# Performance work log

Measured on AMD Instinct MI355X. Metric: run time of the kernel, lower is better.

The kernel has to match this reference:

```python
import jax, jax.numpy as jnp
import numpy as np


def _conv(x, w):
    # 3x3 conv, stride 1, pad 1, NCHW / OIHW
    return jax.lax.conv_general_dilated(
        x, w, window_strides=(1, 1), padding=[(1, 1), (1, 1)],
        dimension_numbers=("NCHW", "OIHW", "NCHW"))


def _up2(x):
    return jnp.repeat(jnp.repeat(x, 2, axis=2), 2, axis=3)


def setup_inputs() -> dict:
    key = jax.random.key(0)
    ks = jax.random.split(key, 16)
    B, S = 8, 256
    d = {
        "x": jax.random.normal(ks[0], (B, 256, 64, 64), jnp.float32),
        "enc1": jax.random.normal(ks[1], (B, 64, 256, 256), jnp.float32),
        "enc2": jax.random.normal(ks[2], (B, 128, 128, 128), jnp.float32),
        "enc3": jax.random.normal(ks[3], (B, 256, 64, 64), jnp.float32),
        "style": jax.random.normal(ks[4], (B, S), jnp.float32),
        # modconv1: 512 -> 128 (bias unused in original F.conv2d call)
        "w1": jax.random.normal(ks[5], (128, 512, 3, 3), jnp.float32) * 0.02,
        "fc_w1": jax.random.normal(ks[6], (128, S), jnp.float32) * 0.05,
        "fc_b1": jax.random.normal(ks[7], (128,), jnp.float32) * 0.05,
        # modconv2: 256 -> 64
        "w2": jax.random.normal(ks[8], (64, 256, 3, 3), jnp.float32) * 0.02,
        "fc_w2": jax.random.normal(ks[9], (64, S), jnp.float32) * 0.05,
        "fc_b2": jax.random.normal(ks[10], (64,), jnp.float32) * 0.05,
        # final_conv: 128 -> 64 -> 3, with biases
        "fw1": jax.random.normal(ks[11], (64, 128, 3, 3), jnp.float32) * 0.02,
        "fb1": jax.random.normal(ks[12], (64,), jnp.float32) * 0.02,
        "fw2": jax.random.normal(ks[13], (3, 64, 3, 3), jnp.float32) * 0.02,
        "fb2": jax.random.normal(ks[14], (3,), jnp.float32) * 0.02,
    }
    return d


def _modconv(x, style, w, fc_w, fc_b):
    # style modulation scales each OUTPUT channel of the conv weight:
    # conv(x, w * s[o]) == s[o] * conv(x, w)  (linearity), so fuse into a
    # single batched conv followed by a per-channel scale.
    s = style @ fc_w.T + fc_b          # [B, out_ch]
    return _conv(x, w) * s[:, :, None, None]


def reference(x, enc1, enc2, enc3, style,
              w1, fc_w1, fc_b1, w2, fc_w2, fc_b2,
              fw1, fb1, fw2, fb2):
    h = jnp.concatenate([x, enc3], axis=1)            # [B,512,64,64]
    h = _up2(h)                                       # [B,512,128,128]
    h = jax.nn.relu(_modconv(h, style, w1, fc_w1, fc_b1))  # [B,128,128,128]
    h = jnp.concatenate([h, enc2], axis=1)            # [B,256,128,128]
    h = _up2(h)                                       # [B,256,256,256]
    h = jax.nn.relu(_modconv(h, style, w2, fc_w2, fc_b2))  # [B,64,256,256]
    h = jnp.concatenate([h, enc1], axis=1)            # [B,128,256,256]
    h = jax.nn.relu(_conv(h, fw1) + fb1[None, :, None, None])
    h = _conv(h, fw2) + fb2[None, :, None, None]      # [B,3,256,256]
    return h
```

## Files before the change

kernel.cpp:

```cpp
#include <hip/hip_runtime.h>
#include <hip/hip_bf16.h>
#include <cstdint>
#include <cstddef>

typedef short short8 __attribute__((ext_vector_type(8)));
typedef unsigned short ushort8 __attribute__((ext_vector_type(8)));
typedef float f32x4 __attribute__((ext_vector_type(4)));

#define DI __device__ __forceinline__

DI float bf2f(__hip_bfloat16 h) { return __bfloat162float(h); }
DI unsigned short f2bf(float f) {
    __hip_bfloat16 h = __float2bfloat16(f);
    return *(unsigned short*)&h;
}

constexpr int cilog2(int v) { int r = 0; while (v > 1) { v >>= 1; ++r; } return r; }

__global__ void detect_dtype(const unsigned short* __restrict__ raw,
                             int* __restrict__ flag) {
    __shared__ int cnt;
    if (threadIdx.x == 0) cnt = 0;
    __syncthreads();
    int local = 0;
    for (int i = threadIdx.x; i < 1024; i += 256) {
        unsigned short u = raw[2 * i];
        int e = (u >> 7) & 0xFF;
        if (e >= 110 && e <= 132) local++;
    }
    atomicAdd(&cnt, local);
    __syncthreads();
    if (threadIdx.x == 0) *flag = (cnt < 512) ? 1 : 0;
}

__global__ void cvt_pad_f32(const void* __restrict__ in, float* __restrict__ out,
                            int n, int npad, const int* __restrict__ flag) {
    int i = blockIdx.x * blockDim.x + threadIdx.x;
    if (i >= npad) return;
    float v = 0.f;
    if (i < n) v = (*flag) ? ((const float*)in)[i] : bf2f(((const __hip_bfloat16*)in)[i]);
    out[i] = v;
}

__global__ void style_mod(const void* __restrict__ style, const void* __restrict__ fcw,
                          const void* __restrict__ fcb, float* __restrict__ out,
                          int B, int O, int S, const int* __restrict__ flag) {
    int i = blockIdx.x * blockDim.x + threadIdx.x;
    if (i >= B * O) return;
    int b = i / O, o = i - b * O;
    float acc = 0.f;
    if (*flag) {
        const float* sp = (const float*)style + (size_t)b * S;
        const float* wp = (const float*)fcw + (size_t)o * S;
        for (int k = 0; k < S; ++k) acc = fmaf(sp[k], wp[k], acc);
        acc += ((const float*)fcb)[o];
    } else {
        const __hip_bfloat16* sp = (const __hip_bfloat16*)style + (size_t)b * S;
        const __hip_bfloat16* wp = (const __hip_bfloat16*)fcw + (size_t)o * S;
        for (int k = 0; k < S; ++k) acc = fmaf(bf2f(sp[k]), bf2f(wp[k]), acc);
        acc += bf2f(((const __hip_bfloat16*)fcb)[o]);
    }
    out[i] = acc;
}

__global__ __launch_bounds__(256)
void nchw_to_nhwc(const void* __restrict__ in, unsigned short* __restrict__ out,
                  int C, int HW, int CT, int coff, const int* __restrict__ flag) {
    __shared__ float t[32][65];
    const int f32 = flag[0];
    const int pbase = blockIdx.x * 64;
    const int cbase = blockIdx.y * 32;
    const int b = blockIdx.z;
    const size_t ibase = ((size_t)b * C + cbase) * HW + pbase;
#pragma unroll
    for (int i = 0; i < 8; ++i) {
        int e = threadIdx.x + i * 256;
        int c = e >> 6, p = e & 63;
        size_t idx = ibase + (size_t)c * HW + p;
        float v = f32 ? ((const float*)in)[idx] : bf2f(((const __hip_bfloat16*)in)[idx]);
        t[c][p] = v;
    }
    __syncthreads();
#pragma unroll
    for (int i = 0; i < 8; ++i) {
        int e = threadIdx.x + i * 256;
        int p = e >> 5, c = e & 31;
        out[((size_t)b * HW + pbase + p) * CT + coff + cbase + c] = f2bf(t[c][p]);
    }
}

__global__ __launch_bounds__(256)
void pack_w(const void* __restrict__ w, unsigned short* __restrict__ pkw,
            int Creal, int CIN, int NC, int KC, const int* __restrict__ flag) {
    int gid = blockIdx.x * 256 + threadIdx.x;
    int total = 9 * KC * NC * 64;
    if (gid >= total) return;
    const int f32 = flag[0];
    int lane = gid & 63; int q = gid >> 6;
    int nc = q % NC; q /= NC; int tap = q % 9; int kc = q / 9;
    int lm = lane & 15, lk = lane >> 4;
    int n = nc * 16 + lm;
    int kh = tap / 3, kw = tap - kh * 3;
    ushort8 v;
#pragma unroll
    for (int j = 0; j < 8; ++j) {
        int k = kc * 32 + lk * 8 + j;
        float f = 0.f;
        if (n < Creal) {
            size_t si = (((size_t)n * CIN + k) * 3 + kh) * 3 + kw;
            f = f32 ? ((const float*)w)[si] : bf2f(((const __hip_bfloat16*)w)[si]);
        }
        v[j] = f2bf(f);
    }
    *(ushort8*)(pkw + (size_t)gid * 8) = v;
}

template<int CT, int H, int W, bool UP, int NT, int NCT, int EPI, int CTO>
__global__ __launch_bounds__(256, 3)
void conv_tile(const unsigned short* __restrict__ in,
               const unsigned short* __restrict__ pkw,
               const float* __restrict__ sb,
               unsigned short* __restrict__ outp) {
    constexpr int KC = CT / 32;
    constexpr int SH = UP ? H / 2 : H;
    constexpr int SW = UP ? W / 2 : W;
    constexpr int NROW = UP ? 6 : 10;
    constexpr int NCOL = UP ? 18 : 34;
    constexpr int NPIX = NROW * NCOL;
    constexpr int NUNIT = 4 * NPIX;
    constexpr int TILES_X = W / 32;
    constexpr int DCOL = UP ? 8 : 16;

    __shared__ __align__(16) unsigned short inA[NUNIT * 8];
    __shared__ __align__(16) unsigned short wbuf[9 * NT * 512];

    const int tid = threadIdx.x;
    const int wave = tid >> 6, lane = tid & 63;
    const int lm = lane & 15, lk = lane >> 4;
    const int x0 = (blockIdx.x % TILES_X) * 32;
    const int y0 = (blockIdx.x / TILES_X) * 8;
    const int nco0 = blockIdx.y * NT;
    const int b = blockIdx.z;

    const int sy0 = UP ? ((y0 - 1) >> 1) : (y0 - 1);
    const int sx0 = UP ? ((x0 - 1) >> 1) : (x0 - 1);

    const unsigned short* gin = in + (size_t)b * SH * SW * CT;

    f32x4 acc[4][NT];
#pragma unroll
    for (int t = 0; t < 4; ++t)
#pragma unroll
        for (int u = 0; u < NT; ++u)
            acc[t][u] = f32x4{0.f, 0.f, 0.f, 0.f};

    for (int kc = 0; kc < KC; ++kc) {
        __syncthreads();
        for (int u0 = tid; u0 < NUNIT; u0 += 256) {
            int pix = u0 >> 2, j = u0 & 3;
            int sr = pix / NCOL, sc = pix - sr * NCOL;
            int gy = sy0 + sr, gx = sx0 + sc;
            uint4 v = uint4{0u, 0u, 0u, 0u};
            if (gy >= 0 && gy < SH && gx >= 0 && gx < SW)
                v = *(const uint4*)((const char*)gin +
                      ((size_t)(gy * SW + gx) * CT + kc * 32) * 2 + j * 16);
            *(uint4*)((char*)inA + (((j * NROW + sr) * NCOL + sc) << 4)) = v;
        }
        {
            const char* wsrc = (const char*)pkw;
            for (int u0 = tid; u0 < 9 * NT * 64; u0 += 256) {
                int tap = u0 / (NT * 64);
                int rem = u0 - tap * (NT * 64);
                size_t soff = ((size_t)(kc * 9 + tap) * NCT + nco0) * 1024 + (size_t)rem * 16;
                uint4 v = *(const uint4*)(wsrc + soff);
                *(uint4*)((char*)wbuf + (size_t)u0 * 16) = v;
            }
        }
        __syncthreads();
#pragma unroll
        for (int tap = 0; tap < 9; ++tap) {
            const int dy = tap / 3 - 1, dx = tap - (tap / 3) * 3 - 1;
            int srow0, srow1, scol0;
            if (UP) {
                srow0 = ((y0 + 2 * wave + dy) >> 1) - sy0;
                srow1 = ((y0 + 2 * wave + 1 + dy) >> 1) - sy0;
                scol0 = ((x0 + lm + dx) >> 1) - sx0;
            } else {
                srow0 = 2 * wave + dy + 1;
                srow1 = srow0 + 1;
                scol0 = lm + dx + 1;
            }
            const int base0 = (lk * NROW + srow0) * NCOL + scol0;
            const int base1 = (lk * NROW + srow1) * NCOL + scol0;
            short8 afr[4];
            afr[0] = *(const short8*)((const char*)inA + (base0 << 4));
            afr[1] = *(const short8*)((const char*)inA + ((base0 + DCOL) << 4));
            afr[2] = *(const short8*)((const char*)inA + (base1 << 4));
            afr[3] = *(const short8*)((const char*)inA + ((base1 + DCOL) << 4));
#pragma unroll
            for (int u = 0; u < NT; ++u) {
                short8 bfr = *(const short8*)((const char*)wbuf +
                                (((tap * NT + u) * 64 + lane) << 4));
#pragma unroll
                for (int t = 0; t < 4; ++t)
                    acc[t][u] = __builtin_amdgcn_mfma_f32_16x16x32_bf16(
                        afr[t], bfr, acc[t][u], 0, 0, 0);
            }
        }
    }

#pragma unroll
    for (int u = 0; u < NT; ++u) {
        const int co = (nco0 + u) * 16 + lm;
        const float s = (EPI == 0) ? sb[b * (NCT * 16) + co] : sb[co];
#pragma unroll
        for (int t = 0; t < 4; ++t) {
            const int row = y0 + 2 * wave + (t >> 1);
            const int colb = x0 + (t & 1) * 16 + lk * 4;
            const size_t pbase = ((size_t)b * H + row) * W + colb;
#pragma unroll
            for (int rr = 0; rr < 4; ++rr) {
                float v = acc[t][u][rr];
                v = (EPI == 0) ? v * s : v + s;
                v = fmaxf(v, 0.f);
                outp[(pbase + rr) * CTO + co] = f2bf(v);
            }
        }
    }
}

template<int CT, int H, int W, bool UP, int NT, int NC, int KCS, int EPI, int CTO>
__global__ __launch_bounds__(256)
void conv_mfma(const unsigned short* __restrict__ in,
               const unsigned short* __restrict__ pkw,
               const float* __restrict__ sb,
               void* __restrict__ outv,
               const int* __restrict__ flagp) {
    constexpr int KC = CT / 32;
    constexpr int HW = H * W;
    constexpr int LHW = cilog2(HW);
    constexpr int LW = cilog2(W);
    constexpr int SW = UP ? W / 2 : W;
    constexpr int SH = UP ? H / 2 : H;
    constexpr int STAGES = KC / KCS;
    __shared__ __align__(16) unsigned short lds[KCS * NT * 512];

    const int tid = threadIdx.x;
    const int wave = tid >> 6, lane = tid & 63;
    const int lm = lane & 15, lk = lane >> 4;
    const int blkm = blockIdx.x * 256;
    const int nco0 = blockIdx.y * NT;

    int pb[4], py[4], px[4];
#pragma unroll
    for (int t = 0; t < 4; ++t) {
        int P = blkm + wave * 64 + t * 16 + lm;
        pb[t] = P >> LHW;
        int rem = P & (HW - 1);
        py[t] = rem >> LW;
        px[t] = rem & (W - 1);
    }

    f32x4 acc[4][NT];
#pragma unroll
    for (int t = 0; t < 4; ++t)
#pragma unroll
        for (int u = 0; u < NT; ++u)
            acc[t][u] = f32x4{0.f, 0.f, 0.f, 0.f};

    for (int tap = 0; tap < 9; ++tap) {
        const int dy = tap / 3 - 1, dx = tap - (tap / 3) * 3 - 1;
        int ab[4]; bool av[4];
#pragma unroll
        for (int t = 0; t < 4; ++t) {
            int ty = py[t] + dy, tx = px[t] + dx;
            av[t] = (ty >= 0) && (ty < H) && (tx >= 0) && (tx < W);
            int iy = UP ? (ty >> 1) : ty;
            int ix = UP ? (tx >> 1) : tx;
            iy = av[t] ? iy : 0; ix = av[t] ? ix : 0;
            ab[t] = (((pb[t] * SH + iy) * SW + ix) * CT + lk * 8) * 2;
        }
        for (int st = 0; st < STAGES; ++st) {
            const int kc0 = st * KCS;
            __syncthreads();
            {
                constexpr int T16 = KCS * NT * 64;
                const char* pwb = (const char*)pkw;
                for (int f = tid; f < T16; f += 256) {
                    int fb = f * 16;
                    int kcl = fb / (NT * 1024);
                    int rem2 = fb - kcl * (NT * 1024);
                    int soff = (((kc0 + kcl) * 9 + tap) * NC + nco0) * 1024 + rem2;
                    uint4 v = *(const uint4*)(pwb + soff);
                    *(uint4*)((char*)lds + fb) = v;
                }
            }
            __syncthreads();
#pragma unroll 4
            for (int kcl = 0; kcl < KCS; ++kcl) {
                short8 a[4];
#pragma unroll
                for (int t = 0; t < 4; ++t) {
                    uint4 raw = *(const uint4*)((const char*)in + (ab[t] + (kc0 + kcl) * 64));
                    uint4 z = uint4{0u, 0u, 0u, 0u};
                    uint4 sel = av[t] ? raw : z;
                    a[t] = *(short8*)&sel;
                }
#pragma unroll
                for (int u = 0; u < NT; ++u) {
                    short8 bfr = *(short8*)((char*)lds + (kcl * NT + u) * 1024 + lane * 16);
#pragma unroll
                    for (int t = 0; t < 4; ++t)
                        acc[t][u] = __builtin_amdgcn_mfma_f32_16x16x32_bf16(
                            a[t], bfr, acc[t][u], 0, 0, 0);
                }
            }
        }
    }

    const int f32o = flagp[0];
    const int co = lm;
    if (co < 3) {
        const float bias = sb[co];
#pragma unroll
        for (int t = 0; t < 4; ++t) {
            const int Pb = blkm + wave * 64 + t * 16 + lk * 4;
#pragma unroll
            for (int r = 0; r < 4; ++r) {
                const int P = Pb + r;
                const int bb = P >> LHW;
                const int rem = P & (HW - 1);
                const float v = acc[t][0][r] + bias;
                const int oi = (bb * 3 + co) * HW + rem;
                if (f32o) ((float*)outv)[oi] = v;
                else ((unsigned short*)outv)[oi] = f2bf(v);
            }
        }
    }
}

template<int CIN, int CSPLIT, int H, int W, bool UP, int CO_TILE, int EPI,
         bool D0, bool D1, bool DOUT>
__global__ __launch_bounds__(256)
void conv3x3(const void* __restrict__ p0, const void* __restrict__ p1,
             const float* __restrict__ wf, const float* __restrict__ sb,
             void* __restrict__ outv, int Cout, const int* __restrict__ flagp) {
    __shared__ float tile[18 * 20];
    constexpr int SH = UP ? H / 2 : H;
    constexpr int SW = UP ? W / 2 : W;
    constexpr int C0 = CSPLIT;
    constexpr int TX = W / 16;

    const int f32 = __builtin_amdgcn_readfirstlane(flagp[0]);
    const int esz0 = (D0 && f32) ? 4 : 2;
    const int esz1 = (D1 && f32) ? 4 : 2;

    const int tid = threadIdx.x;
    const int tx = tid & 15, ty = tid >> 4;
    const int x0 = (blockIdx.x % TX) * 16;
    const int y0 = (blockIdx.x / TX) * 16;
    const int co0 = blockIdx.y * CO_TILE;
    const int b = blockIdx.z;

    const char* bb0 = (const char*)p0 + (size_t)b * C0 * SH * SW * esz0;
    const char* bb1 = (const char*)p1 + (size_t)b * (CIN - C0) * SH * SW * esz1;

    int ly1 = tid / 18, lx1 = tid - ly1 * 18;
    int yy1 = y0 - 1 + ly1, xx1 = x0 - 1 + lx1;
    bool in1 = (yy1 >= 0) && (yy1 < H) && (xx1 >= 0) && (xx1 < W);
    int sof1 = in1 ? ((UP ? (yy1 >> 1) : yy1) * SW + (UP ? (xx1 >> 1) : xx1)) : 0;
    float* tp1 = tile + ly1 * 20 + lx1;

    int t2 = tid + 256;
    bool has2 = (t2 < 324);
    int t2c = has2 ? t2 : 0;
    int ly2 = t2c / 18, lx2 = t2c - ly2 * 18;
    int yy2 = y0 - 1 + ly2, xx2 = x0 - 1 + lx2;
    bool in2 = has2 && (yy2 >= 0) && (yy2 < H) && (xx2 >= 0) && (xx2 < W);
    int sof2 = in2 ? ((UP ? (yy2 >> 1) : yy2) * SW + (UP ? (xx2 >> 1) : xx2)) : 0;
    float* tp2 = tile + ly2 * 20 + lx2;

    float acc[CO_TILE];
#pragma unroll
    for (int j = 0; j < CO_TILE; ++j) acc[j] = 0.f;
    const float* wbase = wf + (size_t)co0 * CIN * 9;

    for (int ci = 0; ci < CIN; ++ci) {
        bool isP0 = (ci < C0);
        const char* src = isP0 ? bb0 + (size_t)ci * SH * SW * esz0
                               : bb1 + (size_t)(ci - C0) * SH * SW * esz1;
        bool sf = isP0 ? (D0 && f32) : (D1 && f32);
        __syncthreads();
        float v1 = 0.f, v2 = 0.f;
        if (sf) {
            if (in1) v1 = ((const float*)src)[sof1];
            if (in2) v2 = ((const float*)src)[sof2];
        } else {
            if (in1) v1 = bf2f(((const __hip_bfloat16*)src)[sof1]);
            if (in2) v2 = bf2f(((const __hip_bfloat16*)src)[sof2]);
        }
        tp1[0] = v1;
        if (has2) tp2[0] = v2;
        __syncthreads();

        float v[9];
#pragma unroll
        for (int r = 0; r < 3; ++r)
#pragma unroll
            for (int c = 0; c < 3; ++c)
                v[r * 3 + c] = tile[(ty + r) * 20 + tx + c];

        const float* wp = wbase + ci * 9;
#pragma unroll
        for (int j = 0; j < CO_TILE; ++j) {
            const float* w9 = wp + (size_t)j * CIN * 9;
#pragma unroll
            for (int k = 0; k < 9; ++k)
                acc[j] = fmaf(v[k], w9[k], acc[j]);
        }
    }

    const int oy = y0 + ty, ox = x0 + tx;
#pragma unroll
    for (int j = 0; j < CO_TILE; ++j) {
        const int co = co0 + j;
        float val = acc[j];
        if (EPI == 0)      val = fmaxf(val * sb[b * Cout + co], 0.f);
        else if (EPI == 1) val = fmaxf(val + sb[co], 0.f);
        else               val = val + sb[co];
        size_t oidx = (((size_t)b * Cout + co) * H + oy) * W + ox;
        if (DOUT && f32) ((float*)outv)[oidx] = val;
        else ((__hip_bfloat16*)outv)[oidx] = __float2bfloat16(val);
    }
}

extern "C" void kernel_launch(void* const* d_in, const int* in_sizes, int n_in,
                              void* d_out, int out_size, void* d_ws, size_t ws_size,
                              hipStream_t stream) {
    const void* x     = d_in[0];   const void* enc1  = d_in[1];
    const void* enc2  = d_in[2];   const void* enc3  = d_in[3];
    const void* style = d_in[4];
    const void* w1    = d_in[5];   const void* fcw1  = d_in[6];  const void* fcb1 = d_in[7];
    const void* w2    = d_in[8];   const void* fcw2  = d_in[9];  const void* fcb2 = d_in[10];
    const void* fw1   = d_in[11];  const void* fb1   = d_in[12];
    const void* fw2   = d_in[13];  const void* fb2   = d_in[14];
    char* ws = (char*)d_ws;
    auto gb = [](int n) { return (n + 255) / 256; };

    constexpr size_t REQ = 272629760ULL;

    if (ws_size >= REQ) {
        unsigned short* pkw1 = (unsigned short*)(ws + 0);
        unsigned short* pkw2 = (unsigned short*)(ws + 1179648);
        unsigned short* pkw3 = (unsigned short*)(ws + 1474560);
        unsigned short* pkw4 = (unsigned short*)(ws + 1622016);
        float* s1    = (float*)(ws + 1640448);
        float* s2    = (float*)(ws + 1644544);
        float* fb1f  = (float*)(ws + 1646592);
        float* fb2f  = (float*)(ws + 1646848);
        int*   flag  = (int*)(ws + 1646912);
        unsigned short* buf0 = (unsigned short*)(ws + (4u << 20));
        unsigned short* h3   = (unsigned short*)(ws + (4u << 20));
        unsigned short* buf1 = (unsigned short*)(ws + (4u << 20) + 67108864u);
        unsigned short* buf2 = (unsigned short*)(ws + (4u << 20) + 134217728u);

        hipLaunchKernelGGL(detect_dtype, dim3(1), dim3(256), 0, stream,
                           (const unsigned short*)style, flag);

        hipLaunchKernelGGL(nchw_to_nhwc, dim3(64, 8, 8),   dim3(256), 0, stream, x,    buf0, 256, 4096,  512, 0,   flag);
        hipLaunchKernelGGL(nchw_to_nhwc, dim3(64, 8, 8),   dim3(256), 0, stream, enc3, buf0, 256, 4096,  512, 256, flag);
        hipLaunchKernelGGL(nchw_to_nhwc, dim3(256, 4, 8),  dim3(256), 0, stream, enc2, buf1, 128, 16384, 256, 128, flag);
        hipLaunchKernelGGL(nchw_to_nhwc, dim3(1024, 2, 8), dim3(256), 0, stream, enc1, buf2, 64,  65536, 128, 64,  flag);

        hipLaunchKernelGGL(pack_w, dim3(gb(73728)), dim3(256), 0, stream, w1,  pkw1, 128, 512, 8, 16, flag);
        hipLaunchKernelGGL(pack_w, dim3(gb(18432)), dim3(256), 0, stream, w2,  pkw2, 64,  256, 4, 8,  flag);
        hipLaunchKernelGGL(pack_w, dim3(gb(9216)),  dim3(256), 0, stream, fw1, pkw3, 64,  128, 4, 4,  flag);
        hipLaunchKernelGGL(pack_w, dim3(gb(1152)),  dim3(256), 0, stream, fw2, pkw4, 3,   64,  1, 2,  flag);

        hipLaunchKernelGGL(style_mod, dim3(4), dim3(256), 0, stream, style, fcw1, fcb1, s1, 8, 128, 256, flag);
        hipLaunchKernelGGL(style_mod, dim3(2), dim3(256), 0, stream, style, fcw2, fcb2, s2, 8, 64, 256, flag);
        hipLaunchKernelGGL(cvt_pad_f32, dim3(1), dim3(256), 0, stream, fb1, fb1f, 64, 64, flag);
        hipLaunchKernelGGL(cvt_pad_f32, dim3(1), dim3(256), 0, stream, fb2, fb2f, 3, 16, flag);

        hipLaunchKernelGGL((conv_tile<512, 128, 128, true, 4, 8, 0, 256>),
                           dim3(64, 2, 8), dim3(256), 0, stream, buf0, pkw1, s1, buf1);
        hipLaunchKernelGGL((conv_tile<256, 256, 256, true, 4, 4, 0, 128>),
                           dim3(256, 1, 8), dim3(256), 0, stream, buf1, pkw2, s2, buf2);
        hipLaunchKernelGGL((conv_tile<128, 256, 256, false, 4, 4, 1, 64>),
                           dim3(256, 1, 8), dim3(256), 0, stream, buf2, pkw3, fb1f, h3);
        hipLaunchKernelGGL((conv_mfma<64, 256, 256, false, 1, 1, 2, 2, 0>),
                           dim3(2048, 1), dim3(256), 0, stream, h3, pkw4, fb2f, d_out, flag);
        return;
    }

    float* w1f  = (float*)(ws + 0);
    float* w2f  = (float*)(ws + 2359296);
    float* fw1f = (float*)(ws + 2949120);
    float* fw2f = (float*)(ws + 3244032);
    float* s1   = (float*)(ws + 3250944);
    float* s2   = (float*)(ws + 3255040);
    float* fb1f = (float*)(ws + 3257088);
    float* fb2f = (float*)(ws + 3257344);
    int*   flag = (int*)(ws + 3257360);
    __hip_bfloat16* h1 = (__hip_bfloat16*)(ws + (size_t)(4u << 20));
    __hip_bfloat16* h3 = (__hip_bfloat16*)(ws + (size_t)(4u << 20));
    __hip_bfloat16* h2 = (__hip_bfloat16*)(ws + (size_t)(4u << 20) + 67108864u);

    hipLaunchKernelGGL(detect_dtype, dim3(1), dim3(256), 0, stream,
                       (const unsigned short*)style, flag);
    hipLaunchKernelGGL(cvt_pad_f32, dim3(gb(589824)), dim3(256), 0, stream, w1, w1f, 589824, 589824, flag);
    hipLaunchKernelGGL(cvt_pad_f32, dim3(gb(147456)), dim3(256), 0, stream, w2, w2f, 147456, 147456, flag);
    hipLaunchKernelGGL(cvt_pad_f32, dim3(gb(73728)),  dim3(256), 0, stream, fw1, fw1f, 73728, 73728, flag);
    hipLaunchKernelGGL(cvt_pad_f32, dim3(gb(1728)),   dim3(256), 0, stream, fw2, fw2f, 1728, 1728, flag);
    hipLaunchKernelGGL(cvt_pad_f32, dim3(1), dim3(256), 0, stream, fb1, fb1f, 64, 64, flag);
    hipLaunchKernelGGL(cvt_pad_f32, dim3(1), dim3(256), 0, stream, fb2, fb2f, 3, 3, flag);
    hipLaunchKernelGGL(style_mod, dim3(4), dim3(256), 0, stream, style, fcw1, fcb1, s1, 8, 128, 256, flag);
    hipLaunchKernelGGL(style_mod, dim3(2), dim3(256), 0, stream, style, fcw2, fcb2, s2, 8, 64, 256, flag);

    hipLaunchKernelGGL((conv3x3<512, 256, 128, 128, true, 8, 0, true, true, false>),
                       dim3(64, 16, 8), dim3(256), 0, stream, x, enc3, w1f, s1, h1, 128, flag);
    hipLaunchKernelGGL((conv3x3<256, 128, 256, 256, true, 8, 0, false, true, false>),
                       dim3(256, 8, 8), dim3(256), 0, stream, h1, enc2, w2f, s2, h2, 64, flag);
    hipLaunchKernelGGL((conv3x3<128, 64, 256, 256, false, 8, 1, false, true, false>),
                       dim3(256, 8, 8), dim3(256), 0, stream, h2, enc1, fw1f, fb1f, h3, 64, flag);
    hipLaunchKernelGGL((conv3x3<64, 64, 256, 256, false, 3, 2, false, false, true>),
                       dim3(256, 1, 8), dim3(256), 0, stream, h3, h3, fw2f, fb2f, d_out, 3, flag);
}
```

Measured before the change: 912.0 us.

## Exploit nearest upsample parity in conv tiles and tile final 3-channel conv

The upsampling convolutions now compute a 16x32 output tile per block. They load each source-resolution fragment once per channel chunk into registers (4 rows x 3 columns). Every output phase (row/column parity) and tap then reuses these fragments, so the per-tap LDS fragment reads disappear and LDS traffic drops. The cost is a larger accumulator array (8xNT) and launch bounds lowered to 2 blocks per CU. The final 3-output-channel conv switches from the per-tap global-load conv_mfma kernel to the LDS-tiled conv_tile with a special epilogue.

After: 807.2 us. -11.5%, faster.

```diff
diff --git a/kernel.cpp b/kernel.cpp
--- a/kernel.cpp
+++ b/kernel.cpp
@@ -115,21 +115,18 @@
     *(ushort8*)(pkw + (size_t)gid * 8) = v;
 }
 
-template<int CT, int H, int W, bool UP, int NT, int NCT, int EPI, int CTO>
-__global__ __launch_bounds__(256, 3)
-void conv_tile(const unsigned short* __restrict__ in,
-               const unsigned short* __restrict__ pkw,
-               const float* __restrict__ sb,
-               unsigned short* __restrict__ outp) {
+template<int CT, int H, int W, int NT, int NCT, int CTO>
+__global__ __launch_bounds__(256, 2)
+void conv_tile_up(const unsigned short* __restrict__ in,
+                  const unsigned short* __restrict__ pkw,
+                  const float* __restrict__ sb,
+                  unsigned short* __restrict__ outp) {
     constexpr int KC = CT / 32;
-    constexpr int SH = UP ? H / 2 : H;
-    constexpr int SW = UP ? W / 2 : W;
-    constexpr int NROW = UP ? 6 : 10;
-    constexpr int NCOL = UP ? 18 : 34;
+    constexpr int SH = H / 2, SW = W / 2;
+    constexpr int NROW = 10, NCOL = 18;
     constexpr int NPIX = NROW * NCOL;
     constexpr int NUNIT = 4 * NPIX;
     constexpr int TILES_X = W / 32;
-    constexpr int DCOL = UP ? 8 : 16;
 
     __shared__ __align__(16) unsigned short inA[NUNIT * 8];
     __shared__ __align__(16) unsigned short wbuf[9 * NT * 512];
@@ -138,18 +135,18 @@
     const int wave = tid >> 6, lane = tid & 63;
     const int lm = lane & 15, lk = lane >> 4;
     const int x0 = (blockIdx.x % TILES_X) * 32;
-    const int y0 = (blockIdx.x / TILES_X) * 8;
+    const int y0 = (blockIdx.x / TILES_X) * 16;
     const int nco0 = blockIdx.y * NT;
     const int b = blockIdx.z;
 
-    const int sy0 = UP ? ((y0 - 1) >> 1) : (y0 - 1);
-    const int sx0 = UP ? ((x0 - 1) >> 1) : (x0 - 1);
+    const int sy0 = (y0 - 1) >> 1;
+    const int sx0 = (x0 - 1) >> 1;
 
     const unsigned short* gin = in + (size_t)b * SH * SW * CT;
 
-    f32x4 acc[4][NT];
-#pragma unroll
-    for (int t = 0; t < 4; ++t)
+    f32x4 acc[8][NT];
+#pragma unroll
+    for (int t = 0; t < 8; ++t)
 #pragma unroll
         for (int u = 0; u < NT; ++u)
             acc[t][u] = f32x4{0.f, 0.f, 0.f, 0.f};
@@ -166,45 +163,37 @@
                       ((size_t)(gy * SW + gx) * CT + kc * 32) * 2 + j * 16);
             *(uint4*)((char*)inA + (((j * NROW + sr) * NCOL + sc) << 4)) = v;
         }
-        {
-            const char* wsrc = (const char*)pkw;
-            for (int u0 = tid; u0 < 9 * NT * 64; u0 += 256) {
-                int tap = u0 / (NT * 64);
-                int rem = u0 - tap * (NT * 64);
-                size_t soff = ((size_t)(kc * 9 + tap) * NCT + nco0) * 1024 + (size_t)rem * 16;
-                uint4 v = *(const uint4*)(wsrc + soff);
-                *(uint4*)((char*)wbuf + (size_t)u0 * 16) = v;
-            }
+        for (int u0 = tid; u0 < 9 * NT * 64; u0 += 256) {
+            int tap = u0 / (NT * 64);
+            int rem = u0 - tap * (NT * 64);
+            size_t soff = ((size_t)(kc * 9 + tap) * NCT + nco0) * 1024 + (size_t)rem * 16;
+            uint4 v = *(const uint4*)((const char*)pkw + soff);
+            *(uint4*)((char*)wbuf + (size_t)u0 * 16) = v;
         }
         __syncthreads();
+
+        short8 F[4][3];
+#pragma unroll
+        for (int fr = 0; fr < 4; ++fr)
+#pragma unroll
+            for (int wn = 0; wn < 3; ++wn)
+                F[fr][wn] = *(const short8*)((const char*)inA +
+                    ((((lk * NROW + 2 * wave + fr) * NCOL) + lm + wn) << 4));
+
 #pragma unroll
         for (int tap = 0; tap < 9; ++tap) {
             const int dy = tap / 3 - 1, dx = tap - (tap / 3) * 3 - 1;
-            int srow0, srow1, scol0;
-            if (UP) {
-                srow0 = ((y0 + 2 * wave + dy) >> 1) - sy0;
-                srow1 = ((y0 + 2 * wave + 1 + dy) >> 1) - sy0;
-                scol0 = ((x0 + lm + dx) >> 1) - sx0;
-            } else {
-                srow0 = 2 * wave + dy + 1;
-                srow1 = srow0 + 1;
-                scol0 = lm + dx + 1;
-            }
-            const int base0 = (lk * NROW + srow0) * NCOL + scol0;
-            const int base1 = (lk * NROW + srow1) * NCOL + scol0;
-            short8 afr[4];
-            afr[0] = *(const short8*)((const char*)inA + (base0 << 4));
-            afr[1] = *(const short8*)((const char*)inA + ((base0 + DCOL) << 4));
-            afr[2] = *(const short8*)((const char*)inA + (base1 << 4));
-            afr[3] = *(const short8*)((const char*)inA + ((base1 + DCOL) << 4));
 #pragma unroll
             for (int u = 0; u < NT; ++u) {
                 short8 bfr = *(const short8*)((const char*)wbuf +
                                 (((tap * NT + u) * 64 + lane) << 4));
 #pragma unroll
-                for (int t = 0; t < 4; ++t)
-                    acc[t][u] = __builtin_amdgcn_mfma_f32_16x16x32_bf16(
-                        afr[t], bfr, acc[t][u], 0, 0, 0);
+                for (int ro = 0; ro < 4; ++ro)
+#pragma unroll
+                    for (int p = 0; p < 2; ++p)
+                        acc[ro * 2 + p][u] = __builtin_amdgcn_mfma_f32_16x16x32_bf16(
+                            F[(ro + dy + 2) >> 1][(p + dx + 2) >> 1], bfr,
+                            acc[ro * 2 + p][u], 0, 0, 0);
             }
         }
     }
@@ -212,54 +201,50 @@
 #pragma unroll
     for (int u = 0; u < NT; ++u) {
         const int co = (nco0 + u) * 16 + lm;
-        const float s = (EPI == 0) ? sb[b * (NCT * 16) + co] : sb[co];
-#pragma unroll
-        for (int t = 0; t < 4; ++t) {
-            const int row = y0 + 2 * wave + (t >> 1);
-            const int colb = x0 + (t & 1) * 16 + lk * 4;
-            const size_t pbase = ((size_t)b * H + row) * W + colb;
-#pragma unroll
-            for (int rr = 0; rr < 4; ++rr) {
-                float v = acc[t][u][rr];
-                v = (EPI == 0) ? v * s : v + s;
-                v = fmaxf(v, 0.f);
-                outp[(pbase + rr) * CTO + co] = f2bf(v);
+        const float s = sb[b * (NCT * 16) + co];
+#pragma unroll
+        for (int ro = 0; ro < 4; ++ro) {
+            const int row = y0 + 4 * wave + ro;
+#pragma unroll
+            for (int p = 0; p < 2; ++p) {
+#pragma unroll
+                for (int rr = 0; rr < 4; ++rr) {
+                    const int col = x0 + 2 * (lk * 4 + rr) + p;
+                    float v = fmaxf(acc[ro * 2 + p][u][rr] * s, 0.f);
+                    outp[((size_t)(b * H + row) * W + col) * CTO + co] = f2bf(v);
+                }
             }
         }
     }
 }
 
-template<int CT, int H, int W, bool UP, int NT, int NC, int KCS, int EPI, int CTO>
-__global__ __launch_bounds__(256)
-void conv_mfma(const unsigned short* __restrict__ in,
+template<int CT, int H, int W, int NT, int NCT, int EPI, int CTO>
+__global__ __launch_bounds__(256, 3)
+void conv_tile(const unsigned short* __restrict__ in,
                const unsigned short* __restrict__ pkw,
                const float* __restrict__ sb,
                void* __restrict__ outv,
                const int* __restrict__ flagp) {
     constexpr int KC = CT / 32;
-    constexpr int HW = H * W;
-    constexpr int LHW = cilog2(HW);
-    constexpr int LW = cilog2(W);
-    constexpr int SW = UP ? W / 2 : W;
-    constexpr int SH = UP ? H / 2 : H;
-    constexpr int STAGES = KC / KCS;
-    __shared__ __align__(16) unsigned short lds[KCS * NT * 512];
+    constexpr int NROW = 10;
+    constexpr int NCOL = 34;
+    constexpr int NPIX = NROW * NCOL;
+    constexpr int NUNIT = 4 * NPIX;
+    constexpr int TILES_X = W / 32;
+
+    __shared__ __align__(16) unsigned short inA[NUNIT * 8];
+    __shared__ __align__(16) unsigned short wbuf[9 * NT * 512];
 
     const int tid = threadIdx.x;
     const int wave = tid >> 6, lane = tid & 63;
     const int lm = lane & 15, lk = lane >> 4;
-    const int blkm = blockIdx.x * 256;
+    const int x0 = (blockIdx.x % TILES_X) * 32;
+    const int y0 = (blockIdx.x / TILES_X) * 8;
     const int nco0 = blockIdx.y * NT;
-
-    int pb[4], py[4], px[4];
-#pragma unroll
-    for (int t = 0; t < 4; ++t) {
-        int P = blkm + wave * 64 + t * 16 + lm;
-        pb[t] = P >> LHW;
-        int rem = P & (HW - 1);
-        py[t] = rem >> LW;
-        px[t] = rem & (W - 1);
-    }
+    const int b = blockIdx.z;
+
+    const int sy0 = y0 - 1, sx0 = x0 - 1;
+    const unsigned short* gin = in + (size_t)b * H * W * CT;
 
     f32x4 acc[4][NT];
 #pragma unroll
@@ -268,72 +253,85 @@
         for (int u = 0; u < NT; ++u)
             acc[t][u] = f32x4{0.f, 0.f, 0.f, 0.f};
 
-    for (int tap = 0; tap < 9; ++tap) {
-        const int dy = tap / 3 - 1, dx = tap - (tap / 3) * 3 - 1;
-        int ab[4]; bool av[4];
-#pragma unroll
-        for (int t = 0; t < 4; ++t) {
-            int ty = py[t] + dy, tx = px[t] + dx;
-            av[t] = (ty >= 0) && (ty < H) && (tx >= 0) && (tx < W);
-            int iy = UP ? (ty >> 1) : ty;
-            int ix = UP ? (tx >> 1) : tx;
-            iy = av[t] ? iy : 0; ix = av[t] ? ix : 0;
-            ab[t] = (((pb[t] * SH + iy) * SW + ix) * CT + lk * 8) * 2;
-        }
-        for (int st = 0; st < STAGES; ++st) {
-            const int kc0 = st * KCS;
-            __syncthreads();
-            {
-                constexpr int T16 = KCS * NT * 64;
-                const char* pwb = (const char*)pkw;
-                for (int f = tid; f < T16; f += 256) {
-                    int fb = f * 16;
-                    int kcl = fb / (NT * 1024);
-                    int rem2 = fb - kcl * (NT * 1024);
-                    int soff = (((kc0 + kcl) * 9 + tap) * NC + nco0) * 1024 + rem2;
-                    uint4 v = *(const uint4*)(pwb + soff);
-                    *(uint4*)((char*)lds + fb) = v;
+    for (int kc = 0; kc < KC; ++kc) {
+        __syncthreads();
+        for (int u0 = tid; u0 < NUNIT; u0 += 256) {
+            int pix = u0 >> 2, j = u0 & 3;
+            int sr = pix / NCOL, sc = pix - sr * NCOL;
+            int gy = sy0 + sr, gx = sx0 + sc;
+            uint4 v = uint4{0u, 0u, 0u, 0u};
+            if (gy >= 0 && gy < H && gx >= 0 && gx < W)
+                v = *(const uint4*)((const char*)gin +
+                      ((size_t)(gy * W + gx) * CT + kc * 32) * 2 + j * 16);
+            *(uint4*)((char*)inA + (((j * NROW + sr) * NCOL + sc) << 4)) = v;
+        }
+        for (int u0 = tid; u0 < 9 * NT * 64; u0 += 256) {
+            int tap = u0 / (NT * 64);
+            int rem = u0 - tap * (NT * 64);
+            size_t soff = ((size_t)(kc * 9 + tap) * NCT + nco0) * 1024 + (size_t)rem * 16;
+            uint4 v = *(const uint4*)((const char*)pkw + soff);
+            *(uint4*)((char*)wbuf + (size_t)u0 * 16) = v;
+        }
+        __syncthreads();
+
+#pragma unroll
+        for (int tap = 0; tap < 9; ++tap) {
+            const int dy = tap / 3 - 1, dx = tap - (tap / 3) * 3 - 1;
+            const int srow0 = 2 * wave + dy + 1;
+            const int scol0 = lm + dx + 1;
+            const int base0 = (lk * NROW + srow0) * NCOL + scol0;
+            const int base1 = (lk * NROW + srow0 + 1) * NCOL + scol0;
+            short8 afr[4];
+            afr[0] = *(const short8*)((const char*)inA + (base0 << 4));
+            afr[1] = *(const short8*)((const char*)inA + ((base0 + 16) << 4));
+            afr[2] = *(const short8*)((const char*)inA + (base1 << 4));
+            afr[3] = *(const short8*)((const char*)inA + ((base1 + 16) << 4));
+#pragma unroll
+            for (int u = 0; u < NT; ++u) {
+                short8 bfr = *(const short8*)((const char*)wbuf +
+                                (((tap * NT + u) * 64 + lane) << 4));
+#pragma unroll
+                for (int t = 0; t < 4; ++t)
+                    acc[t][u] = __builtin_amdgcn_mfma_f32_16x16x32_bf16(
+                        afr[t], bfr, acc[t][u], 0, 0, 0);
+            }
+        }
+    }
+
+    if constexpr (EPI == 1) {
+        unsigned short* outp = (unsigned short*)outv;
+#pragma unroll
+        for (int u = 0; u < NT; ++u) {
+            const int co = (nco0 + u) * 16 + lm;
+            const float s = sb[co];
+#pragma unroll
+            for (int t = 0; t < 4; ++t) {
+                const int row = y0 + 2 * wave + (t >> 1);
+                const int colb = x0 + (t & 1) * 16 + lk * 4;
+                const size_t pbase = ((size_t)(b * H + row)) * W + colb;
+#pragma unroll
+                for (int rr = 0; rr < 4; ++rr) {
+                    float v = fmaxf(acc[t][u][rr] + s, 0.f);
+                    outp[(pbase + rr) * CTO + co] = f2bf(v);
                 }
             }
-            __syncthreads();
-#pragma unroll 4
-            for (int kcl = 0; kcl < KCS; ++kcl) {
-                short8 a[4];
-#pragma unroll
-                for (int t = 0; t < 4; ++t) {
-                    uint4 raw = *(const uint4*)((const char*)in + (ab[t] + (kc0 + kcl) * 64));
-                    uint4 z = uint4{0u, 0u, 0u, 0u};
-                    uint4 sel = av[t] ? raw : z;
-                    a[t] = *(short8*)&sel;
+        }
+    } else {
+        const int f32o = flagp[0];
+        const int co = lm;
+        if (co < 3) {
+            const float bias = sb[co];
+#pragma unroll
+            for (int t = 0; t < 4; ++t) {
+                const int row = y0 + 2 * wave + (t >> 1);
+                const int colb = x0 + (t & 1) * 16 + lk * 4;
+#pragma unroll
+                for (int rr = 0; rr < 4; ++rr) {
+                    const float v = acc[t][0][rr] + bias;
+                    const size_t oi = ((size_t)(b * 3 + co) * H + row) * W + colb + rr;
+                    if (f32o) ((float*)outv)[oi] = v;
+                    else ((unsigned short*)outv)[oi] = f2bf(v);
                 }
-#pragma unroll
-                for (int u = 0; u < NT; ++u) {
-                    short8 bfr = *(short8*)((char*)lds + (kcl * NT + u) * 1024 + lane * 16);
-#pragma unroll
-                    for (int t = 0; t < 4; ++t)
-                        acc[t][u] = __builtin_amdgcn_mfma_f32_16x16x32_bf16(
-                            a[t], bfr, acc[t][u], 0, 0, 0);
-                }
-            }
-        }
-    }
-
-    const int f32o = flagp[0];
-    const int co = lm;
-    if (co < 3) {
-        const float bias = sb[co];
-#pragma unroll
-        for (int t = 0; t < 4; ++t) {
-            const int Pb = blkm + wave * 64 + t * 16 + lk * 4;
-#pragma unroll
-            for (int r = 0; r < 4; ++r) {
-                const int P = Pb + r;
-                const int bb = P >> LHW;
-                const int rem = P & (HW - 1);
-                const float v = acc[t][0][r] + bias;
-                const int oi = (bb * 3 + co) * HW + rem;
-                if (f32o) ((float*)outv)[oi] = v;
-                else ((unsigned short*)outv)[oi] = f2bf(v);
             }
         }
     }
@@ -482,14 +480,14 @@
         hipLaunchKernelGGL(cvt_pad_f32, dim3(1), dim3(256), 0, stream, fb1, fb1f, 64, 64, flag);
         hipLaunchKernelGGL(cvt_pad_f32, dim3(1), dim3(256), 0, stream, fb2, fb2f, 3, 16, flag);
 
-        hipLaunchKernelGGL((conv_tile<512, 128, 128, true, 4, 8, 0, 256>),
-                           dim3(64, 2, 8), dim3(256), 0, stream, buf0, pkw1, s1, buf1);
-        hipLaunchKernelGGL((conv_tile<256, 256, 256, true, 4, 4, 0, 128>),
-                           dim3(256, 1, 8), dim3(256), 0, stream, buf1, pkw2, s2, buf2);
-        hipLaunchKernelGGL((conv_tile<128, 256, 256, false, 4, 4, 1, 64>),
-                           dim3(256, 1, 8), dim3(256), 0, stream, buf2, pkw3, fb1f, h3);
-        hipLaunchKernelGGL((conv_mfma<64, 256, 256, false, 1, 1, 2, 2, 0>),
-                           dim3(2048, 1), dim3(256), 0, stream, h3, pkw4, fb2f, d_out, flag);
+        hipLaunchKernelGGL((conv_tile_up<512, 128, 128, 4, 8, 256>),
+                           dim3(32, 2, 8), dim3(256), 0, stream, buf0, pkw1, s1, buf1);
+        hipLaunchKernelGGL((conv_tile_up<256, 256, 256, 4, 4, 128>),
+                           dim3(128, 1, 8), dim3(256), 0, stream, buf1, pkw2, s2, buf2);
+        hipLaunchKernelGGL((conv_tile<128, 256, 256, 4, 4, 1, 64>),
+                           dim3(256, 1, 8), dim3(256), 0, stream, buf2, pkw3, fb1f, h3, flag);
+        hipLaunchKernelGGL((conv_tile<64, 256, 256, 1, 1, 2, 16>),
+                           dim3(256, 1, 8), dim3(256), 0, stream, h3, pkw4, fb2f, d_out, flag);
         return;
     }
 
```
